# Kernel optimization log

Hardware: AMD Instinct MI355X
Metric: run time of the kernel (lower is better)

Reference implementation:

```python
import jax, jax.numpy as jnp
import numpy as np

HEADS = 8
DIM_HEAD = 64
EPS = 1e-5  # fp32 eps in ChanLayerNorm


def chan_layer_norm(x, g):
    # x: [b, c, h, w]; normalize over channel dim with biased variance
    mean = jnp.mean(x, axis=1, keepdims=True)
    var = jnp.var(x, axis=1, keepdims=True)
    return (x - mean) * jax.lax.rsqrt(var + EPS) * g[None, :, None, None]


def setup_inputs() -> dict:
    key = jax.random.key(0)
    k1, k2, k3 = jax.random.split(key, 3)
    dim, inner = 512, HEADS * DIM_HEAD
    fmap = jax.random.normal(k1, (16, dim, 64, 64), dtype=jnp.float32)
    # 1x1 conv weights (no bias); scaled like typical init to keep softmax unsaturated
    w_qkv = jax.random.normal(k2, (3 * inner, dim), dtype=jnp.float32) * 0.02
    w_out = jax.random.normal(k3, (dim, inner), dtype=jnp.float32) * 0.02
    g1 = jnp.ones((dim,), dtype=jnp.float32)
    g2 = jnp.ones((dim,), dtype=jnp.float32)
    return {"fmap": fmap, "g1": g1, "w_qkv": w_qkv, "w_out": w_out, "g2": g2}


def reference(fmap, g1, w_qkv, w_out, g2):
    b, c, X, Y = fmap.shape
    h, dh = HEADS, DIM_HEAD
    n = X * Y  # seq_len
    scale = dh ** -0.5

    x = chan_layer_norm(fmap, g1)
    # 1x1 conv == channel matmul: [b, 3*inner, X, Y]
    qkv = jnp.einsum('bcxy,oc->boxy', x, w_qkv)
    q, k, v = jnp.split(qkv, 3, axis=1)

    def to_bhnc(t):
        # b (h c) x y -> b h n c
        return t.reshape(b, h, dh, n).transpose(0, 1, 3, 2)

    q, k, v = map(to_bhnc, (q, k, v))

    q = jax.nn.softmax(q, axis=-1) * scale          # softmax over feature dim
    k = jax.nn.softmax(k, axis=2)                   # softmax over seq dim
    v = v / jnp.linalg.norm(v, axis=-1, keepdims=True)  # l2norm
    inv_sqrt_n = 1.0 / np.sqrt(n)
    k = k * inv_sqrt_n
    v = v * inv_sqrt_n

    context = jnp.einsum('bhnd,bhne->bhde', k, v)   # small d x e context
    out = jnp.einsum('bhnd,bhde->bhne', q, context)  # [b, h, n, dh]

    # b h n d -> b (h d) x y
    out = out.transpose(0, 1, 3, 2).reshape(b, h * dh, X, Y)
    out = jax.nn.gelu(out, approximate=False)
    out = jnp.einsum('bcxy,oc->boxy', out, w_out)
    return chan_layer_norm(out, g2)
```

## Files before the change

### kernel.cpp

```cpp
#include <hip/hip_runtime.h>

typedef unsigned short u16;
typedef __attribute__((ext_vector_type(2))) float f32x2;
typedef __attribute__((ext_vector_type(4))) float f32x4;
typedef __attribute__((ext_vector_type(8))) short s16x8;
typedef __attribute__((ext_vector_type(8))) u16 u16x8;
typedef __attribute__((ext_vector_type(4))) u16 u16x4;

#define NB 16
#define CD 512
#define NS 4096
#define NHD 8

#define SBAR  __builtin_amdgcn_s_barrier()
#define SCHED __builtin_amdgcn_sched_barrier(0)
#define PRIO1 __builtin_amdgcn_s_setprio(1)
#define PRIO0 __builtin_amdgcn_s_setprio(0)

__device__ __forceinline__ float bf2f(u16 u){
  union { unsigned int i; float f; } z; z.i = ((unsigned int)u) << 16; return z.f;
}
__device__ __forceinline__ u16 f2bf(float f){
  union { float f; unsigned int i; } z; z.f = f;
  unsigned int i = z.i;
  return (u16)((i + 0x7fffu + ((i >> 16) & 1u)) >> 16);
}
__device__ __forceinline__ float gelu_f(float x){
  return 0.5f * x * (1.0f + erff(x * 0.70710678118654752440f));
}
__device__ __forceinline__ void gl_lds16(const u16* g, u16* l){
  __builtin_amdgcn_global_load_lds((const __attribute__((address_space(1))) void*)(g),
                                   (__attribute__((address_space(3))) void*)(l), 16, 0, 0);
}

__global__ void prep_w_k(const float* __restrict__ wqkv, const float* __restrict__ g1,
                         const float* __restrict__ wout, u16* __restrict__ w1b,
                         u16* __restrict__ w2b){
  int i = blockIdx.x * 256 + threadIdx.x;
  if (i < 1536*512) {
    w1b[i] = f2bf(wqkv[i] * g1[i & 511]);
  } else {
    int j = i - 1536*512;
    w2b[j] = f2bf(wout[j]);
  }
}

__global__ __launch_bounds__(512) void ln1t_k(const float* __restrict__ fmap,
                                              u16* __restrict__ xlnT){
  int b = blockIdx.y, n0 = blockIdx.x * 32;
  int t = threadIdx.x;
  int lane = t & 63, wv = t >> 6;
  __shared__ u16 Lb[512][40];
  __shared__ u16 Tt[64][36];
  __shared__ float red1[8][8][4], red2[8][8][4];
  __shared__ float mean_s[32], rstd_s[32];

  int ng = t & 7;
  float s1[4] = {0,0,0,0}, s2[4] = {0,0,0,0};
  const float* fb = fmap + ((size_t)b*CD)*NS + n0 + ng*4;
  #pragma unroll
  for (int it = 0; it < 8; ++it){
    int q = it*512 + t;
    int c = q >> 3;
    f32x4 v = *(const f32x4*)&fb[(size_t)c*NS];
    u16x4 pk;
    #pragma unroll
    for (int j = 0; j < 4; ++j){
      pk[j] = f2bf(v[j]);
      s1[j] += v[j]; s2[j] += v[j]*v[j];
    }
    *(u16x4*)&Lb[c][ng*4] = pk;
  }
  #pragma unroll
  for (int off = 8; off < 64; off <<= 1)
    #pragma unroll
    for (int j = 0; j < 4; ++j){
      s1[j] += __shfl_xor(s1[j], off, 64);
      s2[j] += __shfl_xor(s2[j], off, 64);
    }
  if (lane < 8){
    #pragma unroll
    for (int j = 0; j < 4; ++j){ red1[wv][lane][j] = s1[j]; red2[wv][lane][j] = s2[j]; }
  }
  __syncthreads();
  if (t < 32){
    int g = t >> 2, j = t & 3;
    float a = 0.f, bq = 0.f;
    #pragma unroll
    for (int w = 0; w < 8; ++w){ a += red1[w][g][j]; bq += red2[w][g][j]; }
    float mn = a * (1.f/512.f);
    float var = bq * (1.f/512.f) - mn*mn;
    mean_s[t] = mn; rstd_s[t] = rsqrtf(var + 1e-5f);
  }
  __syncthreads();

  for (int ct = 0; ct < 8; ++ct){
    {
      int cl = t >> 3, n4 = (t & 7) * 4;
      u16x4 xv = *(const u16x4*)&Lb[ct*64 + cl][n4];
      u16x4 pk;
      #pragma unroll
      for (int j = 0; j < 4; ++j)
        pk[j] = f2bf((bf2f(xv[j]) - mean_s[n4+j]) * rstd_s[n4+j]);
      *(u16x4*)&Tt[cl][n4] = pk;
    }
    __syncthreads();
    {
      int nr = t >> 4, c4 = t & 15;
      u16x4 w;
      #pragma unroll
      for (int j = 0; j < 4; ++j) w[j] = Tt[c4*4 + j][nr];
      *(u16x4*)&xlnT[((size_t)b*NS + n0 + nr)*CD + ct*64 + c4*4] = w;
    }
    __syncthreads();
  }
}

__global__ __launch_bounds__(512) void gemm1q_k(const u16* __restrict__ A,
                                                const u16* __restrict__ Bm,
                                                u16* __restrict__ Q){
  __shared__ u16 lds[8][8192];
  int bi = blockIdx.x;
  int xcd = bi & 7, r2 = bi >> 3;
  int yy = r2 & 1, gi = r2 >> 1;
  int g  = gi*8 + xcd;
  int x  = g & 15, z = g >> 4;
  int o0 = yy*256, bn0 = x*256;
  int t = threadIdx.x;
  int lane = t & 63, wv = t >> 6;
  int wm = wv >> 2, wn = wv & 3;
  int fr = lane & 15, fg = lane >> 4;
  const u16* Ab = A + (size_t)o0*512;
  const u16* Bb = Bm + ((size_t)z*NS + bn0)*512;
  int li8 = lane >> 3, scn = lane & 7;

  f32x4 acc[8][4];
  #pragma unroll
  for (int i=0;i<8;++i)
    #pragma unroll
    for (int j=0;j<4;++j) acc[i][j] = (f32x4){0.f,0.f,0.f,0.f};
  s16x8 afr[4][2];
  s16x8 bfr[2][2][2];

  auto stH = [&](int slot, int half, int kt){
    #pragma unroll
    for (int it=0; it<2; ++it){
      int li = it*64 + wv*8 + li8;
      int q  = scn ^ (li & 7);
      int row;
      if (half < 2) row = ((li>>6)<<7) + half*64 + (li & 63);
      else          row = ((li>>5)<<6) + (half-2)*32 + (li & 31);
      const u16* G = (half < 2) ? Ab : Bb;
      gl_lds16(G + (size_t)row*512 + kt + q*8, &lds[slot*4+half][it*4096 + wv*512]);
    }
  };
  auto ldA = [&](int slot, int mq){
    #pragma unroll
    for (int mr=0;mr<4;++mr)
      #pragma unroll
      for (int ks=0;ks<2;++ks){
        int li = wm*64 + mr*16 + fr;
        int c8 = (ks*4+fg) ^ (li & 7);
        afr[mr][ks] = *(const s16x8*)&lds[slot*4+mq][li*64 + c8*8];
      }
  };
  auto ldB = [&](int slot, int nq){
    #pragma unroll
    for (int nr=0;nr<2;++nr)
      #pragma unroll
      for (int ks=0;ks<2;++ks){
        int li = wn*32 + nr*16 + fr;
        int c8 = (ks*4+fg) ^ (li & 7);
        bfr[nq][nr][ks] = *(const s16x8*)&lds[slot*4+2+nq][li*64 + c8*8];
      }
  };
  auto mm = [&](int mq, int nq){
    #pragma unroll
    for (int mr=0;mr<4;++mr)
      #pragma unroll
      for (int nr=0;nr<2;++nr)
        #pragma unroll
        for (int ks=0;ks<2;++ks)
          acc[mq*4+mr][nq*2+nr] = __builtin_amdgcn_mfma_f32_16x16x32_bf16(
              afr[mr][ks], bfr[nq][nr][ks], acc[mq*4+mr][nq*2+nr], 0,0,0);
  };

  stH(0,0,0); stH(0,2,0); stH(0,3,0); stH(0,1,0);
  asm volatile("s_waitcnt vmcnt(2)" ::: "memory");
  SBAR; SCHED;

  #pragma unroll
  for (int kt=0; kt<8; ++kt){
    int slot = kt & 1, ns = slot ^ 1, kn = (kt+1)*64;
    bool F = kt < 7;
    ldA(slot,0); ldB(slot,0); ldB(slot,1);
    if (F){ stH(ns,0,kn); stH(ns,2,kn); stH(ns,3,kn); }
    PRIO1; mm(0,0); mm(0,1); PRIO0;
    if (F) asm volatile("s_waitcnt vmcnt(6)" ::: "memory");
    else   asm volatile("s_waitcnt vmcnt(0)" ::: "memory");
    SBAR; SCHED;
    ldA(slot,1);
    if (F) stH(ns,1,kn);
    PRIO1; mm(1,1); mm(1,0); PRIO0;
    if (F) asm volatile("s_waitcnt vmcnt(2)" ::: "memory");
    SBAR; SCHED;
  }

  size_t cb = (size_t)z * 512 * NS;
  #pragma unroll
  for (int mq=0;mq<2;++mq)
    #pragma unroll
    for (int mr=0;mr<4;++mr)
      #pragma unroll
      for (int nq=0;nq<2;++nq)
        #pragma unroll
        for (int nr=0;nr<2;++nr){
          int row = o0 + wm*128 + mq*64 + mr*16 + fg*4;
          int col = bn0 + wn*64 + nq*32 + nr*16 + fr;
          #pragma unroll
          for (int r=0;r<4;++r)
            Q[cb + (size_t)(row+r)*NS + col] = f2bf(acc[mq*4+mr][nq*2+nr][r]);
        }
}

__global__ __launch_bounds__(512) void gemm1kv_k(const u16* __restrict__ A,
                                                 const u16* __restrict__ Bm,
                                                 float* __restrict__ part,
                                                 float* __restrict__ mS){
  __shared__ u16 lds[8][8192];
  int bi = blockIdx.x;
  int xcd = bi & 7, r2 = bi >> 3;
  int hp = r2 & 3, gg = r2 >> 2;
  int g8 = gg*8 + xcd;
  int x  = g8 & 15, z = g8 >> 4;
  int bn0 = x*256;
  int t = threadIdx.x;
  int lane = t & 63, wv = t >> 6;
  int wm = wv >> 2, wn = wv & 3;
  int fr = lane & 15, fg = lane >> 4;
  const u16* Akb = A + (size_t)(512  + hp*128)*512;
  const u16* Avb = A + (size_t)(1024 + hp*128)*512;
  const u16* Bb  = Bm + ((size_t)z*NS + bn0)*512;
  int li8 = lane >> 3, scn = lane & 7;

  f32x4 acc[8][4];
  #pragma unroll
  for (int i=0;i<8;++i)
    #pragma unroll
    for (int j=0;j<4;++j) acc[i][j] = (f32x4){0.f,0.f,0.f,0.f};
  s16x8 afr[4][2];
  s16x8 bfr[2][2][2];

  auto stH = [&](int slot, int half, int kt){
    #pragma unroll
    for (int it=0; it<2; ++it){
      int li = it*64 + wv*8 + li8;
      int q  = scn ^ (li & 7);
      if (half < 2){
        int rr = half*64 + (li & 63);
        const u16* G = it ? Avb : Akb;
        gl_lds16(G + (size_t)rr*512 + kt + q*8, &lds[slot*4+half][it*4096 + wv*512]);
      } else {
        int row = ((li>>5)<<6) + (half-2)*32 + (li & 31);
        gl_lds16(Bb + (size_t)row*512 + kt + q*8, &lds[slot*4+half][it*4096 + wv*512]);
      }
    }
  };
  auto ldA = [&](int slot, int mq){
    #pragma unroll
    for (int mr=0;mr<4;++mr)
      #pragma unroll
      for (int ks=0;ks<2;++ks){
        int li = wm*64 + mr*16 + fr;
        int c8 = (ks*4+fg) ^ (li & 7);
        afr[mr][ks] = *(const s16x8*)&lds[slot*4+mq][li*64 + c8*8];
      }
  };
  auto ldB = [&](int slot, int nq){
    #pragma unroll
    for (int nr=0;nr<2;++nr)
      #pragma unroll
      for (int ks=0;ks<2;++ks){
        int li = wn*32 + nr*16 + fr;
        int c8 = (ks*4+fg) ^ (li & 7);
        bfr[nq][nr][ks] = *(const s16x8*)&lds[slot*4+2+nq][li*64 + c8*8];
      }
  };
  auto mm = [&](int mq, int nq){
    #pragma unroll
    for (int mr=0;mr<4;++mr)
      #pragma unroll
      for (int nr=0;nr<2;++nr)
        #pragma unroll
        for (int ks=0;ks<2;++ks)
          acc[mq*4+mr][nq*2+nr] = __builtin_amdgcn_mfma_f32_16x16x32_bf16(
              afr[mr][ks], bfr[nq][nr][ks], acc[mq*4+mr][nq*2+nr], 0,0,0);
  };

  stH(0,0,0); stH(0,2,0); stH(0,3,0); stH(0,1,0);
  asm volatile("s_waitcnt vmcnt(2)" ::: "memory");
  SBAR; SCHED;

  #pragma unroll
  for (int kt=0; kt<8; ++kt){
    int slot = kt & 1, ns = slot ^ 1, kn = (kt+1)*64;
    bool F = kt < 7;
    ldA(slot,0); ldB(slot,0); ldB(slot,1);
    if (F){ stH(ns,0,kn); stH(ns,2,kn); stH(ns,3,kn); }
    PRIO1; mm(0,0); mm(0,1); PRIO0;
    if (F) asm volatile("s_waitcnt vmcnt(6)" ::: "memory");
    else   asm volatile("s_waitcnt vmcnt(0)" ::: "memory");
    SBAR; SCHED;
    ldA(slot,1);
    if (F) stH(ns,1,kn);
    PRIO1; mm(1,1); mm(1,0); PRIO0;
    if (F) asm volatile("s_waitcnt vmcnt(2)" ::: "memory");
    SBAR; SCHED;
  }

  if (wm == 0){
    #pragma unroll
    for (int mq=0;mq<2;++mq)
      #pragma unroll
      for (int mr=0;mr<4;++mr)
        #pragma unroll
        for (int nj=0;nj<4;++nj){
          int nq = nj>>1, nr = nj&1;
          #pragma unroll
          for (int r=0;r<4;++r){
            int d  = mr*16 + fg*4 + r;
            int nl = wn*64 + nq*32 + nr*16 + fr;
            int hh = nl >> 7, n1 = nl & 127;
            lds[mq*2+hh][d*128 + (n1 ^ ((d&7)<<3))] = f2bf(__expf(acc[mq*4+mr][nj][r]));
          }
        }
  } else {
    float ss[2][4];
    #pragma unroll
    for (int mq=0;mq<2;++mq)
      #pragma unroll
      for (int nj=0;nj<4;++nj){
        float s = 0.f;
        #pragma unroll
        for (int mr=0;mr<4;++mr)
          #pragma unroll
          for (int r=0;r<4;++r){ float v = acc[mq*4+mr][nj][r]; s += v*v; }
        s += __shfl_xor(s, 16, 64);
        s += __shfl_xor(s, 32, 64);
        ss[mq][nj] = rsqrtf(s);
      }
    #pragma unroll
    for (int mq=0;mq<2;++mq)
      #pragma unroll
      for (int mr=0;mr<4;++mr)
        #pragma unroll
        for (int nj=0;nj<4;++nj){
          int nq = nj>>1, nr = nj&1;
          #pragma unroll
          for (int r=0;r<4;++r){
            int e  = mr*16 + fg*4 + r;
            int nl = wn*64 + nq*32 + nr*16 + fr;
            int hh = nl >> 7, n1 = nl & 127;
            lds[4 + mq*2+hh][e*128 + (n1 ^ ((e&7)<<3))] = f2bf(acc[mq*4+mr][nj][r] * ss[mq][nj]);
          }
        }
  }
  __syncthreads();

  int eg = wv >> 2, ej = wv & 3, ksl = ej & 1;
  const u16* KTt = &lds[eg*2 + (ej>>1)][0];
  const u16* VTt = &lds[4 + eg*2 + (ej>>1)][0];
  f32x4 a2[4][4];
  #pragma unroll
  for (int i=0;i<4;++i)
    #pragma unroll
    for (int j=0;j<4;++j) a2[i][j] = (f32x4){0.f,0.f,0.f,0.f};
  #pragma unroll
  for (int ks2=0; ks2<2; ++ks2){
    int kc = ksl*64 + ks2*32 + fg*8;
    s16x8 af[4], bf_[4];
    #pragma unroll
    for (int i=0;i<4;++i){
      int ra = i*16 + fr;
      af[i]  = *(const s16x8*)&KTt[ra*128 + (kc ^ ((ra&7)<<3))];
      bf_[i] = *(const s16x8*)&VTt[ra*128 + (kc ^ ((ra&7)<<3))];
    }
    #pragma unroll
    for (int i=0;i<4;++i)
      #pragma unroll
      for (int j=0;j<4;++j)
        a2[i][j] = __builtin_amdgcn_mfma_f32_16x16x32_bf16(af[i], bf_[j], a2[i][j], 0,0,0);
  }
  float slc = 0.f;
  {
    int d = lane;
    #pragma unroll
    for (int cc=0; cc<8; ++cc){
      int c0 = ksl*64 + cc*8;
      u16x8 vv = *(const u16x8*)&KTt[d*128 + (c0 ^ ((d&7)<<3))];
      #pragma unroll
      for (int jj=0;jj<8;++jj) slc += bf2f(vv[jj]);
    }
  }
  __syncthreads();

  if (ej >= 1){
    float* dbuf = (float*)&lds[eg*3 + (ej-1)][0];
    #pragma unroll
    for (int i=0;i<4;++i)
      #pragma unroll
      for (int j=0;j<4;++j)
        #pragma unroll
        for (int r=0;r<4;++r) dbuf[((i*4+j)*4+r)*64 + lane] = a2[i][j][r];
  }
  ((float*)&lds[6][0])[eg*256 + ej*64 + lane] = slc;
  __syncthreads();

  int bh = z*8 + hp*2 + eg;
  size_t base = (size_t)bh*16 + x;
  if (ej == 0){
    #pragma unroll
    for (int bb=0; bb<3; ++bb){
      float* dbuf = (float*)&lds[eg*3 + bb][0];
      #pragma unroll
      for (int i=0;i<4;++i)
        #pragma unroll
        for (int j=0;j<4;++j)
          #pragma unroll
          for (int r=0;r<4;++r) a2[i][j][r] += dbuf[((i*4+j)*4+r)*64 + lane];
    }
    float* pp = part + base*4096;
    #pragma unroll
    for (int i=0;i<4;++i)
      #pragma unroll
      for (int j=0;j<4;++j)
        #pragma unroll
        for (int r=0;r<4;++r)
          pp[(i*16+fg*4+r)*64 + j*16+fr] = a2[i][j][r];
  } else if (ej == 1){
    float* sB = (float*)&lds[6][0];
    float s = sB[eg*256 + lane] + sB[eg*256 + 64 + lane]
            + sB[eg*256 + 128 + lane] + sB[eg*256 + 192 + lane];
    mS[base*128 + lane]      = 0.0f;
    mS[base*128 + 64 + lane] = s;
  }
}

__global__ void ctxred_k(const float* __restrict__ part, const float* __restrict__ mS,
                         float* __restrict__ ctx){
  int bh = blockIdx.x, t = threadIdx.x;
  __shared__ float fs[16][64];
  if (t < 64){
    int d = t;
    float denom = 0.f;
    #pragma unroll
    for (int c=0;c<16;++c)
      denom += mS[((size_t)bh*16 + c)*128 + 64 + d];
    float inv = 1.0f / (denom * 4096.0f);
    #pragma unroll
    for (int c=0;c<16;++c) fs[c][d] = inv;
  }
  __syncthreads();
  #pragma unroll
  for (int i=0;i<16;++i){
    int idx = t + i*256;
    int d = idx >> 6;
    float s = 0.f;
    #pragma unroll
    for (int ch=0; ch<16; ++ch) s += fs[ch][d] * part[((size_t)bh*16 + ch)*4096 + idx];
    ctx[(size_t)bh*4096 + idx] = s;
  }
}

__global__ __launch_bounds__(512) void gemm2f_k(const u16* __restrict__ A,
                                                const u16* __restrict__ q,
                                                const float* __restrict__ ctx,
                                                const float* __restrict__ g2,
                                                float* __restrict__ out){
  __shared__ u16 Ar[2][16384];
  __shared__ u16 Bh[2][4096];
  __shared__ u16 P[128][72];
  __shared__ u16 cT[64][72];
  __shared__ float invP[128];
  int x = blockIdx.x, z = blockIdx.y;
  int n0 = x*128;
  int t = threadIdx.x;
  int lane = t & 63, wv = t >> 6;
  int wm = wv >> 1, wn = wv & 1;
  int wn2 = wv >> 2, we = wv & 3;
  int fr = lane & 15, fg = lane >> 4;
  int l8 = lane >> 3, c8d = lane & 7;
  const u16* Ab = A;

  f32x4 acc[8][4];
  #pragma unroll
  for (int i=0;i<8;++i)
    #pragma unroll
    for (int j=0;j<4;++j) acc[i][j] = (f32x4){0.f,0.f,0.f,0.f};
  s16x8 afr[4], bfr[4];

  auto stA4 = [&](int slot, int kt){
    #pragma unroll
    for (int bt=0; bt<4; ++bt){
      int L  = bt*64 + wv*8 + l8;
      int qq = c8d ^ (l8 & 7);
      int r  = (qq >> 2)*256 + L;
      int col = kt + (qq & 3)*8;
      gl_lds16(Ab + (size_t)r*512 + col, &Ar[slot][(bt*64 + wv*8)*64]);
    }
  };
  auto ldA = [&](int slot, int h2){
    #pragma unroll
    for (int mi=0;mi<4;++mi){
      int R = wm*128 + (h2*4+mi)*16 + fr;
      int L = R & 255, half = R >> 8;
      int c8 = (half*4 + fg) ^ (L & 7);
      afr[mi] = *(const s16x8*)&Ar[slot][L*64 + c8*8];
    }
  };
  auto ldBh = [&](int kt2){
    #pragma unroll
    for (int nj=0;nj<4;++nj){
      int R = wn*64 + nj*16 + fr;
      int L = R & 63, half = R >> 6;
      int c8 = (half*4 + fg) ^ (L & 7);
      bfr[nj] = *(const s16x8*)&Bh[kt2][L*64 + c8*8];
    }
  };
  auto mm16 = [&](int h2){
    #pragma unroll
    for (int mi=0;mi<4;++mi)
      #pragma unroll
      for (int nj=0;nj<4;++nj)
        acc[h2*4+mi][nj] = __builtin_amdgcn_mfma_f32_16x16x32_bf16(
            afr[mi], bfr[nj], acc[h2*4+mi][nj], 0,0,0);
  };

  stA4(0, 0);

  for (int h = 0; h < 8; ++h){
    const float* cs = ctx + ((size_t)(z*8 + h))*4096;
    #pragma unroll
    for (int i=0;i<8;++i){
      int idx = i*512 + t;
      cT[idx & 63][idx >> 6] = f2bf(cs[idx]);
    }
    {
      int nl = wv*16 + (lane & 15);
      int dg = lane >> 4;
      const u16* qb = q + ((size_t)(z*512 + h*64 + dg*16))*NS + n0 + nl;
      float p[16];
      float m = -3.0e38f;
      #pragma unroll
      for (int j=0;j<16;++j){ p[j] = bf2f(qb[(size_t)j*NS]); m = fmaxf(m, p[j]); }
      m = fmaxf(m, __shfl_xor(m, 16, 64));
      m = fmaxf(m, __shfl_xor(m, 32, 64));
      float s = 0.f;
      #pragma unroll
      for (int j=0;j<16;++j){ p[j] = __expf(p[j]-m); s += p[j]; }
      s += __shfl_xor(s, 16, 64);
      s += __shfl_xor(s, 32, 64);
      u16x8 pk;
      #pragma unroll
      for (int j=0;j<8;++j) pk[j] = f2bf(p[j]);
      *(u16x8*)&P[nl][dg*16] = pk;
      #pragma unroll
      for (int j=0;j<8;++j) pk[j] = f2bf(p[8+j]);
      *(u16x8*)&P[nl][dg*16+8] = pk;
      if (dg == 0) invP[nl] = 0.125f / s;
    }
    __syncthreads();
    stA4(1, (2*h+1)*32);

    f32x4 a2[4];
    #pragma unroll
    for (int i=0;i<4;++i) a2[i] = (f32x4){0.f,0.f,0.f,0.f};
    #pragma unroll
    for (int ks=0; ks<2; ++ks){
      s16x8 bfx = *(const s16x8*)&cT[we*16 + fr][ks*32 + fg*8];
      #pragma unroll
      for (int nf=0; nf<4; ++nf){
        s16x8 afx = *(const s16x8*)&P[wn2*64 + nf*16 + fr][ks*32 + fg*8];
        a2[nf] = __builtin_amdgcn_mfma_f32_16x16x32_bf16(afx, bfx, a2[nf], 0,0,0);
      }
    }
    {
      int kt2w = we >> 1;
      #pragma unroll
      for (int nf=0; nf<4; ++nf)
        #pragma unroll
        for (int r=0; r<4; ++r){
          int nl2 = wn2*64 + nf*16 + fg*4 + r;
          int e = we*16 + fr;
          int col = e & 31;
          int L = nl2 & 63;
          int c8 = ((nl2>>6)*4 + (col>>3)) ^ (L & 7);
          Bh[kt2w][L*64 + c8*8 + (col&7)] = f2bf(gelu_f(a2[nf][r] * invP[nl2]));
        }
    }
    asm volatile("s_waitcnt vmcnt(4)" ::: "memory");
    __syncthreads();
    ldA(0,0); ldBh(0);
    PRIO1; mm16(0); PRIO0;
    ldA(0,1);
    PRIO1; mm16(1); PRIO0;
    asm volatile("s_waitcnt vmcnt(0)" ::: "memory");
    __syncthreads();
    if (h < 7) stA4(0, (2*h+2)*32);
    ldA(1,0); ldBh(1);
    PRIO1; mm16(0); PRIO0;
    ldA(1,1);
    PRIO1; mm16(1); PRIO0;
  }

  __syncthreads();
  float* red1 = (float*)&Ar[0][0];
  float* red2 = red1 + 512;
  float* ms   = red2 + 512;
  float* rs   = ms + 128;
  float s1[4], s2[4];
  #pragma unroll
  for (int nj=0;nj<4;++nj){
    float a = 0.f, b2 = 0.f;
    #pragma unroll
    for (int mi=0;mi<8;++mi)
      #pragma unroll
      for (int r=0;r<4;++r){ float v = acc[mi][nj][r]; a += v; b2 += v*v; }
    s1[nj] = a; s2[nj] = b2;
  }
  #pragma unroll
  for (int off=16; off<64; off<<=1)
    #pragma unroll
    for (int nj=0;nj<4;++nj){
      s1[nj] += __shfl_xor(s1[nj], off, 64);
      s2[nj] += __shfl_xor(s2[nj], off, 64);
    }
  if (fg == 0){
    #pragma unroll
    for (int nj=0;nj<4;++nj){
      int c = wn*64 + nj*16 + fr;
      red1[wm*128 + c] = s1[nj];
      red2[wm*128 + c] = s2[nj];
    }
  }
  __syncthreads();
  if (t < 128){
    float a  = red1[t] + red1[128+t] + red1[256+t] + red1[384+t];
    float b2 = red2[t] + red2[128+t] + red2[256+t] + red2[384+t];
    float mn = a * (1.f/512.f);
    float var = b2 * (1.f/512.f) - mn*mn;
    ms[t] = mn; rs[t] = rsqrtf(var + 1e-5f);
  }
  __syncthreads();
  float mc[4], rc[4];
  #pragma unroll
  for (int nj=0;nj<4;++nj){
    int c = wn*64 + nj*16 + fr;
    mc[nj] = ms[c]; rc[nj] = rs[c];
  }
  float* ob = out + (size_t)z*CD*NS + n0;
  #pragma unroll
  for (int mi=0;mi<8;++mi)
    #pragma unroll
    for (int r=0;r<4;++r){
      int row = wm*128 + mi*16 + fg*4 + r;
      float gg = g2[row];
      #pragma unroll
      for (int nj=0;nj<4;++nj)
        ob[(size_t)row*NS + wn*64 + nj*16 + fr] = (acc[mi][nj][r] - mc[nj])*rc[nj]*gg;
    }
}

extern "C" void kernel_launch(void* const* d_in, const int* in_sizes, int n_in,
                              void* d_out, int out_size, void* d_ws, size_t ws_size,
                              hipStream_t stream) {
  const float* fmap = (const float*)d_in[0];
  const float* g1   = (const float*)d_in[1];
  const float* wqkv = (const float*)d_in[2];
  const float* wout = (const float*)d_in[3];
  const float* g2   = (const float*)d_in[4];
  float* out = (float*)d_out;

  char* ws = (char*)d_ws;
  size_t off = 0;
  auto alloc = [&](size_t bytes) -> void* {
    void* p = ws + off;
    off += (bytes + 255) & ~(size_t)255;
    return p;
  };
  u16*   q    = (u16*)alloc((size_t)16*512*4096*2);
  u16*   xlnT = (u16*)alloc((size_t)16*4096*512*2);
  float* part = (float*)alloc((size_t)128*16*4096*4);
  float* mS   = (float*)alloc((size_t)128*16*128*4);
  float* ctx  = (float*)alloc((size_t)128*4096*4);
  u16*   w1b  = (u16*)alloc((size_t)1536*512*2);
  u16*   w2b  = (u16*)alloc((size_t)512*512*2);
  if (off > ws_size) return;

  prep_w_k<<<4096, 256, 0, stream>>>(wqkv, g1, wout, w1b, w2b);
  ln1t_k<<<dim3(128,16), 512, 0, stream>>>(fmap, xlnT);
  gemm1q_k<<<512, 512, 0, stream>>>(w1b, xlnT, q);
  gemm1kv_k<<<1024, 512, 0, stream>>>(w1b, xlnT, part, mS);
  ctxred_k<<<128, 256, 0, stream>>>(part, mS, ctx);
  gemm2f_k<<<dim3(32,16), 512, 0, stream>>>(w2b, q, ctx, g2, out);
}
```

Before: 287.5 us.

## Drop LDS staging of output weights in gemm2f and target two blocks per CU

The double-buffered LDS tile of the output-projection weights is removed, and A fragments are now read straight from global memory (L2-resident weights) inside the MFMA loop. This shrinks shared memory so that, together with launch_bounds(512,2), two blocks can share a CU to hide latency. The context-times-q MFMA tiling is rearranged so each wave writes the GELU results to the B tile with vectorized 4-wide stores instead of scalar stores. The risks are exposed global-load latency on every MFMA step and register pressure under the tighter bound: the 128-float accumulator may spill.

```diff
diff --git a/kernel.cpp b/kernel.cpp
--- a/kernel.cpp
+++ b/kernel.cpp
@@ -472,12 +472,11 @@
   }
 }
 
-__global__ __launch_bounds__(512) void gemm2f_k(const u16* __restrict__ A,
-                                                const u16* __restrict__ q,
-                                                const float* __restrict__ ctx,
-                                                const float* __restrict__ g2,
-                                                float* __restrict__ out){
-  __shared__ u16 Ar[2][16384];
+__global__ __launch_bounds__(512, 2) void gemm2f_k(const u16* __restrict__ A,
+                                                   const u16* __restrict__ q,
+                                                   const float* __restrict__ ctx,
+                                                   const float* __restrict__ g2,
+                                                   float* __restrict__ out){
   __shared__ u16 Bh[2][4096];
   __shared__ u16 P[128][72];
   __shared__ u16 cT[64][72];
@@ -487,9 +486,8 @@
   int t = threadIdx.x;
   int lane = t & 63, wv = t >> 6;
   int wm = wv >> 1, wn = wv & 1;
-  int wn2 = wv >> 2, we = wv & 3;
+  int we2 = wv >> 2, nn = wv & 3;
   int fr = lane & 15, fg = lane >> 4;
-  int l8 = lane >> 3, c8d = lane & 7;
   const u16* Ab = A;
 
   f32x4 acc[8][4];
@@ -499,31 +497,19 @@
     for (int j=0;j<4;++j) acc[i][j] = (f32x4){0.f,0.f,0.f,0.f};
   s16x8 afr[4], bfr[4];
 
-  auto stA4 = [&](int slot, int kt){
-    #pragma unroll
-    for (int bt=0; bt<4; ++bt){
-      int L  = bt*64 + wv*8 + l8;
-      int qq = c8d ^ (l8 & 7);
-      int r  = (qq >> 2)*256 + L;
-      int col = kt + (qq & 3)*8;
-      gl_lds16(Ab + (size_t)r*512 + col, &Ar[slot][(bt*64 + wv*8)*64]);
-    }
-  };
-  auto ldA = [&](int slot, int h2){
+  auto ldAg = [&](int h, int kt2, int h2){
     #pragma unroll
     for (int mi=0;mi<4;++mi){
       int R = wm*128 + (h2*4+mi)*16 + fr;
-      int L = R & 255, half = R >> 8;
-      int c8 = (half*4 + fg) ^ (L & 7);
-      afr[mi] = *(const s16x8*)&Ar[slot][L*64 + c8*8];
+      afr[mi] = *(const s16x8*)&Ab[(size_t)R*512 + h*64 + kt2*32 + fg*8];
     }
   };
   auto ldBh = [&](int kt2){
     #pragma unroll
     for (int nj=0;nj<4;++nj){
       int R = wn*64 + nj*16 + fr;
-      int L = R & 63, half = R >> 6;
-      int c8 = (half*4 + fg) ^ (L & 7);
+      int L = R & 63, hh = R >> 6;
+      int c8 = (hh*4 + fg) ^ (L & 7);
       bfr[nj] = *(const s16x8*)&Bh[kt2][L*64 + c8*8];
     }
   };
@@ -536,8 +522,6 @@
             afr[mi], bfr[nj], acc[h2*4+mi][nj], 0,0,0);
   };
 
-  stA4(0, 0);
-
   for (int h = 0; h < 8; ++h){
     const float* cs = ctx + ((size_t)(z*8 + h))*4096;
     #pragma unroll
@@ -546,9 +530,8 @@
       cT[idx & 63][idx >> 6] = f2bf(cs[idx]);
     }
     {
-      int nl = wv*16 + (lane & 15);
-      int dg = lane >> 4;
-      const u16* qb = q + ((size_t)(z*512 + h*64 + dg*16))*NS + n0 + nl;
+      int nl = wv*16 + fr;
+      const u16* qb = q + ((size_t)(z*512 + h*64 + fg*16))*NS + n0 + nl;
       float p[16];
       float m = -3.0e38f;
       #pragma unroll
@@ -563,58 +546,61 @@
       u16x8 pk;
       #pragma unroll
       for (int j=0;j<8;++j) pk[j] = f2bf(p[j]);
-      *(u16x8*)&P[nl][dg*16] = pk;
+      *(u16x8*)&P[nl][fg*16] = pk;
       #pragma unroll
       for (int j=0;j<8;++j) pk[j] = f2bf(p[8+j]);
-      *(u16x8*)&P[nl][dg*16+8] = pk;
-      if (dg == 0) invP[nl] = 0.125f / s;
+      *(u16x8*)&P[nl][fg*16+8] = pk;
+      if (fg == 0) invP[nl] = 0.125f / s;
     }
     __syncthreads();
-    stA4(1, (2*h+1)*32);
-
-    f32x4 a2[4];
-    #pragma unroll
-    for (int i=0;i<4;++i) a2[i] = (f32x4){0.f,0.f,0.f,0.f};
+
+    f32x4 a2[2][2];
+    #pragma unroll
+    for (int i=0;i<2;++i)
+      #pragma unroll
+      for (int j=0;j<2;++j) a2[i][j] = (f32x4){0.f,0.f,0.f,0.f};
     #pragma unroll
     for (int ks=0; ks<2; ++ks){
-      s16x8 bfx = *(const s16x8*)&cT[we*16 + fr][ks*32 + fg*8];
-      #pragma unroll
-      for (int nf=0; nf<4; ++nf){
-        s16x8 afx = *(const s16x8*)&P[wn2*64 + nf*16 + fr][ks*32 + fg*8];
-        a2[nf] = __builtin_amdgcn_mfma_f32_16x16x32_bf16(afx, bfx, a2[nf], 0,0,0);
+      s16x8 afx[2], bfx[2];
+      #pragma unroll
+      for (int ei=0;ei<2;++ei)
+        afx[ei] = *(const s16x8*)&cT[we2*32 + ei*16 + fr][ks*32 + fg*8];
+      #pragma unroll
+      for (int ni=0;ni<2;++ni)
+        bfx[ni] = *(const s16x8*)&P[nn*32 + ni*16 + fr][ks*32 + fg*8];
+      #pragma unroll
+      for (int ei=0;ei<2;++ei)
+        #pragma unroll
+        for (int ni=0;ni<2;++ni)
+          a2[ei][ni] = __builtin_amdgcn_mfma_f32_16x16x32_bf16(afx[ei], bfx[ni], a2[ei][ni], 0,0,0);
+    }
+    #pragma unroll
+    for (int ei=0;ei<2;++ei)
+      #pragma unroll
+      for (int ni=0;ni<2;++ni){
+        int n = nn*32 + ni*16 + fr;
+        float ip = invP[n];
+        u16x4 w4;
+        #pragma unroll
+        for (int r=0;r<4;++r) w4[r] = f2bf(gelu_f(a2[ei][ni][r] * ip));
+        int e32 = ei*16 + fg*4;
+        int chunk = e32 >> 3, sub = e32 & 7;
+        int L = n & 63, hh = n >> 6;
+        int c8 = (hh*4 + chunk) ^ (L & 7);
+        *(u16x4*)&Bh[we2][L*64 + c8*8 + sub] = w4;
       }
-    }
-    {
-      int kt2w = we >> 1;
-      #pragma unroll
-      for (int nf=0; nf<4; ++nf)
-        #pragma unroll
-        for (int r=0; r<4; ++r){
-          int nl2 = wn2*64 + nf*16 + fg*4 + r;
-          int e = we*16 + fr;
-          int col = e & 31;
-          int L = nl2 & 63;
-          int c8 = ((nl2>>6)*4 + (col>>3)) ^ (L & 7);
-          Bh[kt2w][L*64 + c8*8 + (col&7)] = f2bf(gelu_f(a2[nf][r] * invP[nl2]));
-        }
-    }
-    asm volatile("s_waitcnt vmcnt(4)" ::: "memory");
     __syncthreads();
-    ldA(0,0); ldBh(0);
-    PRIO1; mm16(0); PRIO0;
-    ldA(0,1);
-    PRIO1; mm16(1); PRIO0;
-    asm volatile("s_waitcnt vmcnt(0)" ::: "memory");
-    __syncthreads();
-    if (h < 7) stA4(0, (2*h+2)*32);
-    ldA(1,0); ldBh(1);
-    PRIO1; mm16(0); PRIO0;
-    ldA(1,1);
-    PRIO1; mm16(1); PRIO0;
-  }
-
-  __syncthreads();
-  float* red1 = (float*)&Ar[0][0];
+
+    #pragma unroll
+    for (int kt2=0; kt2<2; ++kt2){
+      ldBh(kt2);
+      ldAg(h,kt2,0); PRIO1; mm16(0); PRIO0;
+      ldAg(h,kt2,1); PRIO1; mm16(1); PRIO0;
+    }
+  }
+
+  __syncthreads();
+  float* red1 = (float*)&P[0][0];
   float* red2 = red1 + 512;
   float* ms   = red2 + 512;
   float* rs   = ms + 128;
```

Result: slower. 311.6 us (+8.4%).
